# Kernel tuning notes

Hardware: AMD Instinct MI355X
Metric: run time of the kernel (lower is better)

Reference implementation:

```python
import jax, jax.numpy as jnp
import numpy as np

LN_EPS = 1e-5
L2_EPS = 1e-12  # torch F.normalize eps


def _layernorm(h, g, b):
    mu = jnp.mean(h, axis=-1, keepdims=True)
    var = jnp.var(h, axis=-1, keepdims=True)
    return (h - mu) * jax.lax.rsqrt(var + LN_EPS) * g + b


def _l2norm(h):
    n = jnp.linalg.norm(h, axis=-1, keepdims=True)
    return h / jnp.maximum(n, L2_EPS)


def _temperature(epoch, total_epochs):
    warmup = total_epochs * 0.1
    if epoch < warmup:
        return 2.0
    progress = (epoch - warmup) / (total_epochs - warmup)
    return max(0.7, 2.0 - 1.3 * progress)


def setup_inputs() -> dict:
    key = jax.random.key(0)
    ks = jax.random.split(key, 4)
    B, T, D, P, C = 8, 4096, 1024, 512, 64
    x = jax.random.normal(ks[0], (B, T, D), dtype=jnp.float32)
    w1 = jax.random.normal(ks[1], (D, C), dtype=jnp.float32) * 0.02
    b1 = jnp.zeros((C,), jnp.float32)
    ln1_g = jnp.ones((C,), jnp.float32)
    ln1_b = jnp.zeros((C,), jnp.float32)
    patterns = jax.random.normal(ks[2], (P, C), dtype=jnp.float32)
    patterns = _l2norm(patterns)  # init is row-orthonormalized in torch via SVD; unit rows suffice
    w2 = jax.random.normal(ks[3], (C, D), dtype=jnp.float32) * 0.02
    b2 = jnp.zeros((D,), jnp.float32)
    ln2_g = jnp.ones((D,), jnp.float32)
    ln2_b = jnp.zeros((D,), jnp.float32)
    return {"x": x, "w1": w1, "b1": b1, "ln1_g": ln1_g, "ln1_b": ln1_b,
            "patterns": patterns, "w2": w2, "b2": b2, "ln2_g": ln2_g, "ln2_b": ln2_b,
            "epoch": 0, "total_epochs": 100}


def reference(x, w1, b1, ln1_g, ln1_b, patterns, w2, b2, ln2_g, ln2_b, epoch, total_epochs):
    n_patterns = patterns.shape[0]
    # bottleneck projection + LayerNorm: [B,T,D] -> [B,T,C]
    Q = _layernorm(jnp.einsum('btd,dc->btc', x, w1) + b1, ln1_g, ln1_b)
    Q_norm = _l2norm(Q)
    K_norm = _l2norm(patterns)  # [P,C]
    temp = _temperature(epoch, total_epochs)
    logits = jnp.einsum('btc,pc->btp', Q_norm, K_norm) / temp  # [B,T,P]
    hard_indices = jnp.argmax(logits, axis=-1)  # [B,T]
    assignments = jax.nn.one_hot(hard_indices, n_patterns, dtype=jnp.float32)  # eval: hard
    pattern_emb_low = jnp.einsum('btp,pc->btc', assignments, patterns)
    pattern_emb = _layernorm(jnp.einsum('btc,cd->btd', pattern_emb_low, w2) + b2, ln2_g, ln2_b)
    return (pattern_emb, assignments, logits, hard_indices, Q)
```

## Files before the change

kernel.cpp:

```cpp
#include <hip/hip_runtime.h>

#define O_PE 0
#define O_AS 33554432
#define O_LG 50331648
#define O_HI 67108864
#define O_Q  67141632

__global__ void k0_pre(const float* __restrict__ patterns, const float* __restrict__ w2,
                       const float* __restrict__ b2, const float* __restrict__ ln2g,
                       const float* __restrict__ ln2b, const int* __restrict__ epoch,
                       const int* __restrict__ total_epochs,
                       float* __restrict__ invt, float* __restrict__ knT,
                       float* __restrict__ peb) {
  const int b = blockIdx.x, t = threadIdx.x;
  __shared__ float pat[64];
  __shared__ float red[8];

  if (b == 0 && t == 0) {
    float ep = (float)epoch[0], te = (float)total_epochs[0];
    float warm = te * 0.1f;
    float temp;
    if (ep < warm) temp = 2.0f;
    else {
      float prog = (ep - warm) / (te - warm);
      temp = fmaxf(0.7f, 2.0f - 1.3f * prog);
    }
    invt[0] = 1.0f / temp;
  }

  if (t < 64) pat[t] = patterns[b * 64 + t];
  __syncthreads();

  if (t < 64) {
    float v = pat[t];
    float s = v * v;
    #pragma unroll
    for (int m = 1; m < 64; m <<= 1) s += __shfl_xor(s, m);
    float scale = 1.0f / fmaxf(sqrtf(s), 1e-12f);
    knT[(size_t)t * 512 + b] = v * scale;
  }

  const int d0 = t * 4;
  float4 acc = *(const float4*)&b2[d0];
  #pragma unroll 8
  for (int k = 0; k < 64; ++k) {
    float pk = pat[k];
    float4 w = *(const float4*)&w2[(size_t)k * 1024 + d0];
    acc.x = fmaf(pk, w.x, acc.x);
    acc.y = fmaf(pk, w.y, acc.y);
    acc.z = fmaf(pk, w.z, acc.z);
    acc.w = fmaf(pk, w.w, acc.w);
  }
  float s1 = acc.x + acc.y + acc.z + acc.w;
  float s2 = acc.x*acc.x + acc.y*acc.y + acc.z*acc.z + acc.w*acc.w;
  #pragma unroll
  for (int m = 1; m < 64; m <<= 1) { s1 += __shfl_xor(s1, m); s2 += __shfl_xor(s2, m); }
  const int wid = t >> 6;
  if ((t & 63) == 0) { red[wid] = s1; red[wid + 4] = s2; }
  __syncthreads();
  s1 = red[0] + red[1] + red[2] + red[3];
  s2 = red[4] + red[5] + red[6] + red[7];
  float mu = s1 * (1.0f / 1024.0f);
  float var = s2 * (1.0f / 1024.0f) - mu * mu;
  float rstd = rsqrtf(var + 1e-5f);
  float4 g  = *(const float4*)&ln2g[d0];
  float4 bb = *(const float4*)&ln2b[d0];
  float4 o;
  o.x = (acc.x - mu) * rstd * g.x + bb.x;
  o.y = (acc.y - mu) * rstd * g.y + bb.y;
  o.z = (acc.z - mu) * rstd * g.z + bb.z;
  o.w = (acc.w - mu) * rstd * g.w + bb.w;
  *(float4*)&peb[(size_t)b * 1024 + d0] = o;
}

#define FMA16(AV, BV, A)                              \
  A[0][0] = fmaf(AV.x, BV.x, A[0][0]);                \
  A[0][1] = fmaf(AV.x, BV.y, A[0][1]);                \
  A[0][2] = fmaf(AV.x, BV.z, A[0][2]);                \
  A[0][3] = fmaf(AV.x, BV.w, A[0][3]);                \
  A[1][0] = fmaf(AV.y, BV.x, A[1][0]);                \
  A[1][1] = fmaf(AV.y, BV.y, A[1][1]);                \
  A[1][2] = fmaf(AV.y, BV.z, A[1][2]);                \
  A[1][3] = fmaf(AV.y, BV.w, A[1][3]);                \
  A[2][0] = fmaf(AV.z, BV.x, A[2][0]);                \
  A[2][1] = fmaf(AV.z, BV.y, A[2][1]);                \
  A[2][2] = fmaf(AV.z, BV.z, A[2][2]);                \
  A[2][3] = fmaf(AV.z, BV.w, A[2][3]);                \
  A[3][0] = fmaf(AV.w, BV.x, A[3][0]);                \
  A[3][1] = fmaf(AV.w, BV.y, A[3][1]);                \
  A[3][2] = fmaf(AV.w, BV.z, A[3][2]);                \
  A[3][3] = fmaf(AV.w, BV.w, A[3][3]);

__global__ __launch_bounds__(256, 2) void k1_main(
    const float* __restrict__ x, const float* __restrict__ w1,
    const float* __restrict__ b1, const float* __restrict__ ln1g,
    const float* __restrict__ ln1b, const float* __restrict__ knT,
    const float* __restrict__ invtp,
    float* __restrict__ outQ, float* __restrict__ outLg,
    float* __restrict__ outAs, float* __restrict__ outHi,
    int* __restrict__ idxw) {
  __shared__ float xsT[64][68];
  __shared__ float wks[64][68];
  __shared__ float qnT[64][68];
  __shared__ int   sidx[64];

  const int tid = threadIdx.x;
  const int rowbase = blockIdx.x * 64;
  const int r0 = (tid >> 4) * 4;
  const int c0 = (tid & 15) * 4;

  float acc[4][4] = {{0.f, 0.f, 0.f, 0.f}, {0.f, 0.f, 0.f, 0.f},
                     {0.f, 0.f, 0.f, 0.f}, {0.f, 0.f, 0.f, 0.f}};
  for (int kt = 0; kt < 16; ++kt) {
    const int dbase = kt * 64;
    #pragma unroll
    for (int pass = 0; pass < 4; ++pass) {
      const int rp = (tid >> 4) + pass * 16;
      const int dd = (tid & 15) * 4;
      float4 xv = *(const float4*)&x[(size_t)(rowbase + rp) * 1024 + dbase + dd];
      xsT[dd + 0][rp] = xv.x; xsT[dd + 1][rp] = xv.y;
      xsT[dd + 2][rp] = xv.z; xsT[dd + 3][rp] = xv.w;
      *(float4*)&wks[rp][dd] = *(const float4*)&w1[(size_t)(dbase + rp) * 64 + dd];
    }
    __syncthreads();
    #pragma unroll 8
    for (int k = 0; k < 64; ++k) {
      float4 xv = *(float4*)&xsT[k][r0];
      float4 wv = *(float4*)&wks[k][c0];
      FMA16(xv, wv, acc)
    }
    __syncthreads();
  }

  {
    float4 b1v = *(const float4*)&b1[c0];
    float4 g1v = *(const float4*)&ln1g[c0];
    float4 e1v = *(const float4*)&ln1b[c0];
    #pragma unroll
    for (int i = 0; i < 4; ++i) {
      float h0 = acc[i][0] + b1v.x;
      float h1 = acc[i][1] + b1v.y;
      float h2 = acc[i][2] + b1v.z;
      float h3 = acc[i][3] + b1v.w;
      float s1 = h0 + h1 + h2 + h3;
      float s2 = h0*h0 + h1*h1 + h2*h2 + h3*h3;
      #pragma unroll
      for (int m = 1; m < 16; m <<= 1) { s1 += __shfl_xor(s1, m); s2 += __shfl_xor(s2, m); }
      float mu   = s1 * 0.015625f;
      float var  = s2 * 0.015625f - mu * mu;
      float rstd = rsqrtf(var + 1e-5f);
      float q0 = (h0 - mu) * rstd * g1v.x + e1v.x;
      float q1 = (h1 - mu) * rstd * g1v.y + e1v.y;
      float q2 = (h2 - mu) * rstd * g1v.z + e1v.z;
      float q3 = (h3 - mu) * rstd * g1v.w + e1v.w;
      float t2 = q0*q0 + q1*q1 + q2*q2 + q3*q3;
      #pragma unroll
      for (int m = 1; m < 16; m <<= 1) t2 += __shfl_xor(t2, m);
      float scl = 1.0f / fmaxf(sqrtf(t2), 1e-12f);
      float4 qo; qo.x = q0; qo.y = q1; qo.z = q2; qo.w = q3;
      *(float4*)&outQ[(size_t)(rowbase + r0 + i) * 64 + c0] = qo;
      qnT[c0 + 0][r0 + i] = q0 * scl;
      qnT[c0 + 1][r0 + i] = q1 * scl;
      qnT[c0 + 2][r0 + i] = q2 * scl;
      qnT[c0 + 3][r0 + i] = q3 * scl;
    }
  }

  const float invt = invtp[0];
  float bmax[4]; int bidx[4];
  #pragma unroll
  for (int i = 0; i < 4; ++i) { bmax[i] = -3.0e38f; bidx[i] = 0; }

  for (int pt = 0; pt < 8; ++pt) {
    __syncthreads();
    #pragma unroll
    for (int pass = 0; pass < 4; ++pass) {
      const int cc = (tid >> 4) + pass * 16;
      const int pp = (tid & 15) * 4;
      *(float4*)&wks[cc][pp] = *(const float4*)&knT[(size_t)cc * 512 + pt * 64 + pp];
    }
    __syncthreads();
    float a2[4][4] = {{0.f, 0.f, 0.f, 0.f}, {0.f, 0.f, 0.f, 0.f},
                      {0.f, 0.f, 0.f, 0.f}, {0.f, 0.f, 0.f, 0.f}};
    #pragma unroll 8
    for (int k = 0; k < 64; ++k) {
      float4 qv = *(float4*)&qnT[k][r0];
      float4 kv = *(float4*)&wks[k][c0];
      FMA16(qv, kv, a2)
    }
    #pragma unroll
    for (int i = 0; i < 4; ++i) {
      float v0 = a2[i][0] * invt;
      float v1 = a2[i][1] * invt;
      float v2 = a2[i][2] * invt;
      float v3 = a2[i][3] * invt;
      const int pb = pt * 64 + c0;
      if (v0 > bmax[i]) { bmax[i] = v0; bidx[i] = pb; }
      if (v1 > bmax[i]) { bmax[i] = v1; bidx[i] = pb + 1; }
      if (v2 > bmax[i]) { bmax[i] = v2; bidx[i] = pb + 2; }
      if (v3 > bmax[i]) { bmax[i] = v3; bidx[i] = pb + 3; }
      float4 lo; lo.x = v0; lo.y = v1; lo.z = v2; lo.w = v3;
      *(float4*)&outLg[(size_t)(rowbase + r0 + i) * 512 + pb] = lo;
    }
  }

  #pragma unroll
  for (int i = 0; i < 4; ++i) {
    #pragma unroll
    for (int m = 1; m < 16; m <<= 1) {
      float ov = __shfl_xor(bmax[i], m);
      int   oi = __shfl_xor(bidx[i], m);
      if (ov > bmax[i] || (ov == bmax[i] && oi < bidx[i])) { bmax[i] = ov; bidx[i] = oi; }
    }
  }
  if ((tid & 15) == 0) {
    #pragma unroll
    for (int i = 0; i < 4; ++i) {
      sidx[r0 + i] = bidx[i];
      idxw[rowbase + r0 + i] = bidx[i];
      outHi[rowbase + r0 + i] = (float)bidx[i];
    }
  }
  __syncthreads();

  #pragma unroll
  for (int pass = 0; pass < 32; ++pass) {
    const int ch  = tid + pass * 256;
    const int r   = ch >> 7;
    const int pcc = (ch & 127) * 4;
    const int bi  = sidx[r];
    float4 z; z.x = 0.f; z.y = 0.f; z.z = 0.f; z.w = 0.f;
    if (bi >= pcc && bi < pcc + 4) ((float*)&z)[bi - pcc] = 1.0f;
    *(float4*)&outAs[(size_t)(rowbase + r) * 512 + pcc] = z;
  }
}

__global__ void k3_gather(const float4* __restrict__ peb, const int* __restrict__ idxw,
                          float4* __restrict__ outPe) {
  const int tid = threadIdx.x;
  const int rbase = blockIdx.x * 4;
  #pragma unroll
  for (int pass = 0; pass < 4; ++pass) {
    const int r = rbase + pass;
    const int idx = idxw[r];
    outPe[(size_t)r * 256 + tid] = peb[(size_t)idx * 256 + tid];
  }
}

extern "C" void kernel_launch(void* const* d_in, const int* in_sizes, int n_in,
                              void* d_out, int out_size, void* d_ws, size_t ws_size,
                              hipStream_t stream) {
  (void)in_sizes; (void)n_in; (void)out_size; (void)ws_size;
  const float* x        = (const float*)d_in[0];
  const float* w1       = (const float*)d_in[1];
  const float* b1       = (const float*)d_in[2];
  const float* ln1g     = (const float*)d_in[3];
  const float* ln1b     = (const float*)d_in[4];
  const float* patterns = (const float*)d_in[5];
  const float* w2       = (const float*)d_in[6];
  const float* b2       = (const float*)d_in[7];
  const float* ln2g     = (const float*)d_in[8];
  const float* ln2b     = (const float*)d_in[9];
  const int*   epoch    = (const int*)d_in[10];
  const int*   total    = (const int*)d_in[11];

  float* out = (float*)d_out;
  float* outPe = out + O_PE;
  float* outAs = out + O_AS;
  float* outLg = out + O_LG;
  float* outHi = out + O_HI;
  float* outQ  = out + O_Q;

  float* wsf  = (float*)d_ws;
  float* invt = wsf;
  float* knT  = wsf + 64;
  float* peb  = (float*)((char*)d_ws + 131328);
  int*   idxw = (int*)((char*)d_ws + 2228480);

  hipLaunchKernelGGL(k0_pre, dim3(512), dim3(256), 0, stream,
                     patterns, w2, b2, ln2g, ln2b, epoch, total, invt, knT, peb);
  hipLaunchKernelGGL(k1_main, dim3(512), dim3(256), 0, stream,
                     x, w1, b1, ln1g, ln1b, knT, invt, outQ, outLg, outAs, outHi, idxw);
  hipLaunchKernelGGL(k3_gather, dim3(8192), dim3(256), 0, stream,
                     (const float4*)peb, idxw, (float4*)outPe);
}
```

Baseline: 172.0 us.

## Fuse pattern gather into main kernel and remap work to per-row lanes

The separate gather kernel is folded into the main kernel, which now writes pattern_emb directly from the precomputed per-pattern rows, removing one launch and the index workspace round trip. The main kernel moves to 512 threads: each lane owns one row and each wave owns a slice of channels or patterns. Weight and key values are read wave-uniformly from global memory (likely scalar loads) instead of being staged in shared memory, and the x tile uses an XOR-swizzled layout. LayerNorm and argmax reductions now cross waves through shared memory, and the wave-uniform weight loads may become latency-bound.

Result: slower. 329.8 us (+91.8%).

```diff
diff --git a/kernel.cpp b/kernel.cpp
--- a/kernel.cpp
+++ b/kernel.cpp
@@ -73,177 +73,162 @@
   *(float4*)&peb[(size_t)b * 1024 + d0] = o;
 }
 
-#define FMA16(AV, BV, A)                              \
-  A[0][0] = fmaf(AV.x, BV.x, A[0][0]);                \
-  A[0][1] = fmaf(AV.x, BV.y, A[0][1]);                \
-  A[0][2] = fmaf(AV.x, BV.z, A[0][2]);                \
-  A[0][3] = fmaf(AV.x, BV.w, A[0][3]);                \
-  A[1][0] = fmaf(AV.y, BV.x, A[1][0]);                \
-  A[1][1] = fmaf(AV.y, BV.y, A[1][1]);                \
-  A[1][2] = fmaf(AV.y, BV.z, A[1][2]);                \
-  A[1][3] = fmaf(AV.y, BV.w, A[1][3]);                \
-  A[2][0] = fmaf(AV.z, BV.x, A[2][0]);                \
-  A[2][1] = fmaf(AV.z, BV.y, A[2][1]);                \
-  A[2][2] = fmaf(AV.z, BV.z, A[2][2]);                \
-  A[2][3] = fmaf(AV.z, BV.w, A[2][3]);                \
-  A[3][0] = fmaf(AV.w, BV.x, A[3][0]);                \
-  A[3][1] = fmaf(AV.w, BV.y, A[3][1]);                \
-  A[3][2] = fmaf(AV.w, BV.z, A[3][2]);                \
-  A[3][3] = fmaf(AV.w, BV.w, A[3][3]);
-
-__global__ __launch_bounds__(256, 2) void k1_main(
+__global__ __launch_bounds__(512, 4) void k1_main(
     const float* __restrict__ x, const float* __restrict__ w1,
     const float* __restrict__ b1, const float* __restrict__ ln1g,
     const float* __restrict__ ln1b, const float* __restrict__ knT,
-    const float* __restrict__ invtp,
-    float* __restrict__ outQ, float* __restrict__ outLg,
-    float* __restrict__ outAs, float* __restrict__ outHi,
-    int* __restrict__ idxw) {
-  __shared__ float xsT[64][68];
-  __shared__ float wks[64][68];
-  __shared__ float qnT[64][68];
-  __shared__ int   sidx[64];
+    const float* __restrict__ invtp, const float* __restrict__ peb,
+    float* __restrict__ outPe, float* __restrict__ outAs,
+    float* __restrict__ outLg, float* __restrict__ outHi,
+    float* __restrict__ outQ) {
+  __shared__ float4 xs4[16][64];
+  __shared__ float  qnL[64 * 64];
+  __shared__ float  red1[8][64], red2[8][64], red3[8][64];
+  __shared__ float  avm[8][64];
+  __shared__ int    avi[8][64];
+  __shared__ int    sidx[64];
 
   const int tid = threadIdx.x;
+  const int l   = tid & 63;
+  const int w   = tid >> 6;
+  const int wu  = __builtin_amdgcn_readfirstlane(w);
   const int rowbase = blockIdx.x * 64;
-  const int r0 = (tid >> 4) * 4;
-  const int c0 = (tid & 15) * 4;
-
-  float acc[4][4] = {{0.f, 0.f, 0.f, 0.f}, {0.f, 0.f, 0.f, 0.f},
-                     {0.f, 0.f, 0.f, 0.f}, {0.f, 0.f, 0.f, 0.f}};
+  const size_t row_l = (size_t)(rowbase + l);
+
+  float acc[8];
+  #pragma unroll
+  for (int j = 0; j < 8; ++j) acc[j] = 0.f;
+
+  const int srow = tid >> 4;
+  const int skc  = tid & 15;
+  const float* xrow0 = x + (size_t)(rowbase + srow) * 1024 + skc * 4;
+  const float* xrow1 = xrow0 + (size_t)32 * 1024;
+
   for (int kt = 0; kt < 16; ++kt) {
     const int dbase = kt * 64;
-    #pragma unroll
-    for (int pass = 0; pass < 4; ++pass) {
-      const int rp = (tid >> 4) + pass * 16;
-      const int dd = (tid & 15) * 4;
-      float4 xv = *(const float4*)&x[(size_t)(rowbase + rp) * 1024 + dbase + dd];
-      xsT[dd + 0][rp] = xv.x; xsT[dd + 1][rp] = xv.y;
-      xsT[dd + 2][rp] = xv.z; xsT[dd + 3][rp] = xv.w;
-      *(float4*)&wks[rp][dd] = *(const float4*)&w1[(size_t)(dbase + rp) * 64 + dd];
-    }
+    float4 v0 = *(const float4*)(xrow0 + dbase);
+    float4 v1 = *(const float4*)(xrow1 + dbase);
     __syncthreads();
-    #pragma unroll 8
-    for (int k = 0; k < 64; ++k) {
-      float4 xv = *(float4*)&xsT[k][r0];
-      float4 wv = *(float4*)&wks[k][c0];
-      FMA16(xv, wv, acc)
-    }
+    xs4[skc][srow ^ skc] = v0;
+    xs4[skc][(srow + 32) ^ skc] = v1;
     __syncthreads();
-  }
-
+    #pragma unroll 4
+    for (int kc = 0; kc < 16; ++kc) {
+      float4 xv = xs4[kc][l ^ kc];
+      const float* wp = w1 + (size_t)(dbase + kc * 4) * 64 + wu * 8;
+      float wv0[8], wv1[8], wv2[8], wv3[8];
+      #pragma unroll
+      for (int j = 0; j < 8; ++j) {
+        wv0[j] = wp[j]; wv1[j] = wp[64 + j]; wv2[j] = wp[128 + j]; wv3[j] = wp[192 + j];
+      }
+      #pragma unroll
+      for (int j = 0; j < 8; ++j)
+        acc[j] = fmaf(xv.x, wv0[j],
+                 fmaf(xv.y, wv1[j],
+                 fmaf(xv.z, wv2[j],
+                 fmaf(xv.w, wv3[j], acc[j]))));
+    }
+  }
+
+  float bb[8], gg[8], ee[8];
   {
-    float4 b1v = *(const float4*)&b1[c0];
-    float4 g1v = *(const float4*)&ln1g[c0];
-    float4 e1v = *(const float4*)&ln1b[c0];
-    #pragma unroll
-    for (int i = 0; i < 4; ++i) {
-      float h0 = acc[i][0] + b1v.x;
-      float h1 = acc[i][1] + b1v.y;
-      float h2 = acc[i][2] + b1v.z;
-      float h3 = acc[i][3] + b1v.w;
-      float s1 = h0 + h1 + h2 + h3;
-      float s2 = h0*h0 + h1*h1 + h2*h2 + h3*h3;
-      #pragma unroll
-      for (int m = 1; m < 16; m <<= 1) { s1 += __shfl_xor(s1, m); s2 += __shfl_xor(s2, m); }
-      float mu   = s1 * 0.015625f;
-      float var  = s2 * 0.015625f - mu * mu;
-      float rstd = rsqrtf(var + 1e-5f);
-      float q0 = (h0 - mu) * rstd * g1v.x + e1v.x;
-      float q1 = (h1 - mu) * rstd * g1v.y + e1v.y;
-      float q2 = (h2 - mu) * rstd * g1v.z + e1v.z;
-      float q3 = (h3 - mu) * rstd * g1v.w + e1v.w;
-      float t2 = q0*q0 + q1*q1 + q2*q2 + q3*q3;
-      #pragma unroll
-      for (int m = 1; m < 16; m <<= 1) t2 += __shfl_xor(t2, m);
-      float scl = 1.0f / fmaxf(sqrtf(t2), 1e-12f);
-      float4 qo; qo.x = q0; qo.y = q1; qo.z = q2; qo.w = q3;
-      *(float4*)&outQ[(size_t)(rowbase + r0 + i) * 64 + c0] = qo;
-      qnT[c0 + 0][r0 + i] = q0 * scl;
-      qnT[c0 + 1][r0 + i] = q1 * scl;
-      qnT[c0 + 2][r0 + i] = q2 * scl;
-      qnT[c0 + 3][r0 + i] = q3 * scl;
-    }
-  }
+    const float* bp = b1   + wu * 8;
+    const float* gp = ln1g + wu * 8;
+    const float* ep = ln1b + wu * 8;
+    #pragma unroll
+    for (int j = 0; j < 8; ++j) { bb[j] = bp[j]; gg[j] = gp[j]; ee[j] = ep[j]; }
+  }
+  float h[8]; float ps1 = 0.f, ps2 = 0.f;
+  #pragma unroll
+  for (int j = 0; j < 8; ++j) { h[j] = acc[j] + bb[j]; ps1 += h[j]; ps2 += h[j]*h[j]; }
+  red1[w][l] = ps1; red2[w][l] = ps2;
+  __syncthreads();
+  float s1 = 0.f, s2 = 0.f;
+  #pragma unroll
+  for (int v = 0; v < 8; ++v) { s1 += red1[v][l]; s2 += red2[v][l]; }
+  const float mu   = s1 * 0.015625f;
+  const float var  = s2 * 0.015625f - mu * mu;
+  const float rstd = rsqrtf(var + 1e-5f);
+  float q[8]; float ps = 0.f;
+  #pragma unroll
+  for (int j = 0; j < 8; ++j) { q[j] = (h[j] - mu) * rstd * gg[j] + ee[j]; ps += q[j]*q[j]; }
+  red3[w][l] = ps;
+  {
+    float4 qa; qa.x = q[0]; qa.y = q[1]; qa.z = q[2]; qa.w = q[3];
+    float4 qc; qc.x = q[4]; qc.y = q[5]; qc.z = q[6]; qc.w = q[7];
+    *(float4*)&outQ[row_l * 64 + wu * 8]     = qa;
+    *(float4*)&outQ[row_l * 64 + wu * 8 + 4] = qc;
+  }
+  __syncthreads();
+  float t2 = 0.f;
+  #pragma unroll
+  for (int v = 0; v < 8; ++v) t2 += red3[v][l];
+  const float scl = 1.0f / fmaxf(sqrtf(t2), 1e-12f);
+  #pragma unroll
+  for (int j = 0; j < 8; ++j) qnL[(wu * 8 + j) * 64 + l] = q[j] * scl;
+  __syncthreads();
 
   const float invt = invtp[0];
-  float bmax[4]; int bidx[4];
-  #pragma unroll
-  for (int i = 0; i < 4; ++i) { bmax[i] = -3.0e38f; bidx[i] = 0; }
-
-  for (int pt = 0; pt < 8; ++pt) {
-    __syncthreads();
-    #pragma unroll
-    for (int pass = 0; pass < 4; ++pass) {
-      const int cc = (tid >> 4) + pass * 16;
-      const int pp = (tid & 15) * 4;
-      *(float4*)&wks[cc][pp] = *(const float4*)&knT[(size_t)cc * 512 + pt * 64 + pp];
-    }
-    __syncthreads();
-    float a2[4][4] = {{0.f, 0.f, 0.f, 0.f}, {0.f, 0.f, 0.f, 0.f},
-                      {0.f, 0.f, 0.f, 0.f}, {0.f, 0.f, 0.f, 0.f}};
-    #pragma unroll 8
-    for (int k = 0; k < 64; ++k) {
-      float4 qv = *(float4*)&qnT[k][r0];
-      float4 kv = *(float4*)&wks[k][c0];
-      FMA16(qv, kv, a2)
-    }
-    #pragma unroll
-    for (int i = 0; i < 4; ++i) {
-      float v0 = a2[i][0] * invt;
-      float v1 = a2[i][1] * invt;
-      float v2 = a2[i][2] * invt;
-      float v3 = a2[i][3] * invt;
-      const int pb = pt * 64 + c0;
-      if (v0 > bmax[i]) { bmax[i] = v0; bidx[i] = pb; }
-      if (v1 > bmax[i]) { bmax[i] = v1; bidx[i] = pb + 1; }
-      if (v2 > bmax[i]) { bmax[i] = v2; bidx[i] = pb + 2; }
-      if (v3 > bmax[i]) { bmax[i] = v3; bidx[i] = pb + 3; }
-      float4 lo; lo.x = v0; lo.y = v1; lo.z = v2; lo.w = v3;
-      *(float4*)&outLg[(size_t)(rowbase + r0 + i) * 512 + pb] = lo;
-    }
-  }
-
-  #pragma unroll
-  for (int i = 0; i < 4; ++i) {
-    #pragma unroll
-    for (int m = 1; m < 16; m <<= 1) {
-      float ov = __shfl_xor(bmax[i], m);
-      int   oi = __shfl_xor(bidx[i], m);
-      if (ov > bmax[i] || (ov == bmax[i] && oi < bidx[i])) { bmax[i] = ov; bidx[i] = oi; }
-    }
-  }
-  if ((tid & 15) == 0) {
-    #pragma unroll
-    for (int i = 0; i < 4; ++i) {
-      sidx[r0 + i] = bidx[i];
-      idxw[rowbase + r0 + i] = bidx[i];
-      outHi[rowbase + r0 + i] = (float)bidx[i];
-    }
-  }
-  __syncthreads();
-
-  #pragma unroll
-  for (int pass = 0; pass < 32; ++pass) {
-    const int ch  = tid + pass * 256;
-    const int r   = ch >> 7;
-    const int pcc = (ch & 127) * 4;
-    const int bi  = sidx[r];
+  float bmax = -3.0e38f; int bidx = 0;
+  #pragma unroll
+  for (int pp = 0; pp < 2; ++pp) {
+    const int pbase = wu * 64 + pp * 32;
+    float a2[32];
+    #pragma unroll
+    for (int j = 0; j < 32; ++j) a2[j] = 0.f;
+    #pragma unroll 2
+    for (int c = 0; c < 64; ++c) {
+      const float qv = qnL[c * 64 + l];
+      const float* kp = knT + (size_t)c * 512 + pbase;
+      float kv[32];
+      #pragma unroll
+      for (int j = 0; j < 32; ++j) kv[j] = kp[j];
+      #pragma unroll
+      for (int j = 0; j < 32; ++j) a2[j] = fmaf(qv, kv[j], a2[j]);
+    }
+    #pragma unroll
+    for (int j = 0; j < 32; ++j)
+      if (a2[j] > bmax) { bmax = a2[j]; bidx = pbase + j; }
+    #pragma unroll
+    for (int j4 = 0; j4 < 8; ++j4) {
+      float4 o;
+      o.x = a2[j4*4 + 0] * invt; o.y = a2[j4*4 + 1] * invt;
+      o.z = a2[j4*4 + 2] * invt; o.w = a2[j4*4 + 3] * invt;
+      *(float4*)&outLg[row_l * 512 + pbase + j4 * 4] = o;
+    }
+  }
+
+  avm[w][l] = bmax; avi[w][l] = bidx;
+  __syncthreads();
+  float bm = avm[0][l]; int bi = avi[0][l];
+  #pragma unroll
+  for (int v = 1; v < 8; ++v) {
+    float m = avm[v][l];
+    int   i = avi[v][l];
+    if (m > bm) { bm = m; bi = i; }
+  }
+  if (w == 0) { sidx[l] = bi; outHi[rowbase + l] = (float)bi; }
+  __syncthreads();
+
+  #pragma unroll
+  for (int p = 0; p < 16; ++p) {
+    const int e  = tid + p * 512;
+    const int r  = e >> 7;
+    const int c4 = (e & 127) * 4;
+    const int bi2 = sidx[r];
     float4 z; z.x = 0.f; z.y = 0.f; z.z = 0.f; z.w = 0.f;
-    if (bi >= pcc && bi < pcc + 4) ((float*)&z)[bi - pcc] = 1.0f;
-    *(float4*)&outAs[(size_t)(rowbase + r) * 512 + pcc] = z;
-  }
-}
-
-__global__ void k3_gather(const float4* __restrict__ peb, const int* __restrict__ idxw,
-                          float4* __restrict__ outPe) {
-  const int tid = threadIdx.x;
-  const int rbase = blockIdx.x * 4;
-  #pragma unroll
-  for (int pass = 0; pass < 4; ++pass) {
-    const int r = rbase + pass;
-    const int idx = idxw[r];
-    outPe[(size_t)r * 256 + tid] = peb[(size_t)idx * 256 + tid];
+    if (bi2 >= c4 && bi2 < c4 + 4) ((float*)&z)[bi2 - c4] = 1.0f;
+    *(float4*)&outAs[(size_t)(rowbase + r) * 512 + c4] = z;
+  }
+
+  const float4* peb4 = (const float4*)peb;
+  float4* outPe4 = (float4*)outPe;
+  #pragma unroll
+  for (int p = 0; p < 32; ++p) {
+    const int e  = tid + p * 512;
+    const int r  = e >> 8;
+    const int c4 = e & 255;
+    outPe4[(size_t)(rowbase + r) * 256 + c4] = peb4[(size_t)sidx[r] * 256 + c4];
   }
 }
 
@@ -275,12 +260,10 @@
   float* invt = wsf;
   float* knT  = wsf + 64;
   float* peb  = (float*)((char*)d_ws + 131328);
-  int*   idxw = (int*)((char*)d_ws + 2228480);
 
   hipLaunchKernelGGL(k0_pre, dim3(512), dim3(256), 0, stream,
                      patterns, w2, b2, ln2g, ln2b, epoch, total, invt, knT, peb);
-  hipLaunchKernelGGL(k1_main, dim3(512), dim3(256), 0, stream,
-                     x, w1, b1, ln1g, ln1b, knT, invt, outQ, outLg, outAs, outHi, idxw);
-  hipLaunchKernelGGL(k3_gather, dim3(8192), dim3(256), 0, stream,
-                     (const float4*)peb, idxw, (float4*)outPe);
+  hipLaunchKernelGGL(k1_main, dim3(512), dim3(512), 0, stream,
+                     x, w1, b1, ln1g, ln1b, knT, invt, peb,
+                     outPe, outAs, outLg, outHi, outQ);
 }
```
